# Optimization experiments

Hardware: AMD Instinct MI355X
Metric: run time of the kernel (lower is better)

The kernel has to match this reference:

```python
import jax, jax.numpy as jnp
import numpy as np
import math

B, H, W, CIN = 8, 64, 64, 192
INNER, K, N, P = 384, 2, 32, 64
NHK = INNER // P          # heads per scan direction = 6
NH = K * NHK              # total heads = 12
HID = 4 * CIN

def _silu(v):
    return v * jax.nn.sigmoid(v)

def setup_inputs() -> dict:
    key = jax.random.key(0)
    ks = jax.random.split(key, 12)
    x = jax.random.normal(ks[0], (B, H, W, CIN), jnp.float32)
    W_in = jax.random.normal(ks[1], (2 * INNER, CIN), jnp.float32) * 0.02
    conv_w = jax.random.normal(ks[2], (INNER, 1, 3, 3), jnp.float32) * 0.1
    conv_b = jnp.zeros((INNER,), jnp.float32)
    x_proj_weight = jax.random.normal(ks[3], (K, 2 * N + NHK, INNER), jnp.float32) * 0.02
    A_logs = jnp.log(jax.random.uniform(ks[4], (NH,), jnp.float32, 1.0, 16.0))
    Ds = jnp.ones((NH,), jnp.float32)
    u = jax.random.uniform(ks[5], (NH,), jnp.float32)
    dt = jnp.exp(u * (math.log(0.1) - math.log(0.001)) + math.log(0.001))
    dt = jnp.clip(dt, 1e-4, None)
    dt_bias = dt + jnp.log(-jnp.expm1(-dt))
    init_states = jnp.zeros((NH, P, N), jnp.float32)
    W_out = jax.random.normal(ks[6], (CIN, INNER), jnp.float32) * 0.02
    W1 = jax.random.normal(ks[7], (HID, CIN), jnp.float32) * 0.02
    b1 = jnp.zeros((HID,), jnp.float32)
    W2 = jax.random.normal(ks[8], (CIN, HID), jnp.float32) * 0.02
    b2 = jnp.zeros((CIN,), jnp.float32)
    return dict(x=x, W_in=W_in, conv_w=conv_w, conv_b=conv_b, x_proj_weight=x_proj_weight,
                A_logs=A_logs, Ds=Ds, dt_bias=dt_bias, init_states=init_states,
                W_out=W_out, W1=W1, b1=b1, W2=W2, b2=b2)

def reference(x, W_in, conv_w, conv_b, x_proj_weight, A_logs, Ds, dt_bias,
              init_states, W_out, W1, b1, W2, b2):
    Bb, Hh, Ww, Cin = x.shape
    L = Hh * Ww
    inner = W_in.shape[0] // 2
    shortcut = x
    # norm1 is identity (norm=None). in_proj (no bias), split into x and gate z
    xz = jnp.einsum('bhwc,dc->bhwd', x, W_in)
    xl, z = jnp.split(xz, 2, axis=-1)
    # depthwise conv (NCHW) + SiLU
    xc = jnp.transpose(xl, (0, 3, 1, 2))
    xc = jax.lax.conv_general_dilated(xc, conv_w, (1, 1), 'SAME',
                                      feature_group_count=inner,
                                      dimension_numbers=('NCHW', 'OIHW', 'NCHW'))
    xc = _silu(xc + conv_b[None, :, None, None])
    # cross scan: row-major and transposed (W-major) flattenings
    xs = jnp.stack([xc.reshape(Bb, inner, L),
                    jnp.transpose(xc, (0, 1, 3, 2)).reshape(Bb, inner, L)], axis=1)  # (B,K,inner,L)
    # project to B, C, dt per direction
    BCdt = jnp.einsum('bkdl,kcd->blkc', xs, x_proj_weight)  # (B,L,K,2N+NHK)
    Bs = BCdt[..., :N]                     # (B,L,K,N)
    Cs = BCdt[..., N:2 * N]                # (B,L,K,N)
    dt = BCdt[..., 2 * N:].reshape(Bb, L, NH)
    xh = jnp.transpose(xs, (0, 3, 1, 2)).reshape(Bb, L, NH, P)  # heads: k-major
    # Mamba2 selective scan (dt_softplus with bias)
    dt = jax.nn.softplus(dt + dt_bias)     # (B,L,NH)
    A = -jnp.exp(A_logs)                   # (NH,)
    da = jnp.exp(dt * A)                   # (B,L,NH)
    dtx = dt[..., None] * xh               # (B,L,NH,P)
    Bh = jnp.repeat(Bs, NHK, axis=2)       # (B,L,NH,N) group -> heads
    Ch = jnp.repeat(Cs, NHK, axis=2)
    h0 = jnp.broadcast_to(init_states, (Bb,) + init_states.shape)  # (B,NH,P,N)
    def step(h, inp):
        da_t, dtx_t, B_t, C_t = inp
        h = da_t[..., None, None] * h + dtx_t[..., None] * B_t[:, :, None, :]
        y_t = jnp.einsum('bhpn,bhn->bhp', h, C_t)
        return h, y_t
    _, ys = jax.lax.scan(step, h0, (jnp.moveaxis(da, 1, 0), jnp.moveaxis(dtx, 1, 0),
                                    jnp.moveaxis(Bh, 1, 0), jnp.moveaxis(Ch, 1, 0)))
    y = jnp.moveaxis(ys, 0, 1) + Ds[None, None, :, None] * xh  # (B,L,NH,P)
    out_y = jnp.transpose(y.reshape(Bb, L, K, inner), (0, 2, 3, 1))  # (B,K,inner,L)
    # scan_proj: undo each direction's flattening and sum
    y0 = out_y[:, 0].reshape(Bb, inner, Hh, Ww)
    y1 = jnp.transpose(out_y[:, 1].reshape(Bb, inner, Ww, Hh), (0, 1, 3, 2))
    yr = jnp.transpose((y0 + y1).reshape(Bb, inner, L), (0, 2, 1)).reshape(Bb, Hh, Ww, inner)
    # gate, out_proj, residual, MLP branch (dense is identity since in==out)
    yg = yr * _silu(z)
    out = shortcut + jnp.einsum('bhwd,cd->bhwc', yg, W_out)
    h1 = _silu(jnp.einsum('...c,dc->...d', out, W1) + b1)
    mlp = jnp.einsum('...d,cd->...c', h1, W2) + b2
    return out + mlp
```

## Files before the change

### kernel.cpp

```cpp
#include <hip/hip_runtime.h>
#include <math.h>

#define BB 8
#define HH 64
#define WW 64
#define CIN 192
#define INNER 384
#define LL 4096
#define NSTATE 32
#define PDIM 64
#define NHK 6
#define NHEADS 12
#define HID 768
#define CPROJ 70
#define QC 64
#define NC 64

#define WS_XLZ   0u
#define WS_XC    50331648u
#define WS_Y1    75497472u
#define WS_BCBF  100663296u
#define WS_DTRAW 109051904u
#define WS_DTV   119013376u
#define WS_CUMS  120586240u
#define WS_SHB   122159104u
#define WS_Y0    147324928u
#define WS_XBF   172490752u
#define WS_WINB  185073664u
#define WS_WPADB 185368576u
#define WS_WOUTB 185565184u
#define WS_W1B   185761792u
#define WS_W2B   186056704u
#define WS_REQ   186449920u

typedef __attribute__((ext_vector_type(8))) short short8;
typedef __attribute__((ext_vector_type(4))) float f32x4;

__device__ __forceinline__ float silu_f(float x) { return x / (1.f + __expf(-x)); }

__device__ __forceinline__ unsigned short f2bf(float f) {
    unsigned u = __float_as_uint(f);
    u += 0x7fffu + ((u >> 16) & 1u);
    return (unsigned short)(u >> 16);
}
__device__ __forceinline__ float bf2f(unsigned short u) {
    return __uint_as_float(((unsigned)u) << 16);
}

template<int EPI, int TRANSA>
__global__ __launch_bounds__(256)
void gemm_bf16(const unsigned short* __restrict__ A, const unsigned short* __restrict__ Wt,
               const float* __restrict__ bias, const float* __restrict__ res,
               float* __restrict__ Cf, unsigned short* __restrict__ Cb,
               int Kd, int ldc, int nmax)
{
    __shared__ __align__(16) short Als[128 * 64];
    __shared__ __align__(16) short Bls[128 * 64];
    const int tid = threadIdx.x;
    const int m0 = blockIdx.x * 128;
    const int n0 = blockIdx.y * 128;
    const int lane = tid & 63;
    const int wv = tid >> 6;
    const int wm = (wv >> 1) << 6;
    const int wn = (wv & 1) << 6;

    const unsigned short* gA[4];
    const unsigned short* gB[4];
    int lw[4];
    #pragma unroll
    for (int c = 0; c < 4; ++c) {
        const int idx = c * 256 + tid;
        const int row = idx >> 3;
        const int kb  = idx & 7;
        const int sb  = kb ^ (row & 7);
        lw[c] = row * 64 + sb * 8;
        size_t arow;
        const int mm = m0 + row;
        if (TRANSA) {
            const int bq = mm >> 12, lq = mm & 4095;
            arow = ((size_t)bq << 12) + (size_t)(((lq & 63) << 6) + (lq >> 6));
        } else {
            arow = (size_t)mm;
        }
        gA[c] = A + arow * Kd + kb * 8;
        gB[c] = Wt + (size_t)(n0 + row) * Kd + kb * 8;
    }

    f32x4 acc[4][4];
    #pragma unroll
    for (int i = 0; i < 4; ++i)
        #pragma unroll
        for (int j = 0; j < 4; ++j) acc[i][j] = (f32x4){0.f, 0.f, 0.f, 0.f};

    const int NT = Kd >> 6;
    short8 pA[4], pB[4];
    #pragma unroll
    for (int c = 0; c < 4; ++c) {
        pA[c] = *(const short8*)(gA[c]);
        pB[c] = *(const short8*)(gB[c]);
    }
    for (int kt = 0; kt < NT; ++kt) {
        __syncthreads();
        #pragma unroll
        for (int c = 0; c < 4; ++c) {
            *(short8*)&Als[lw[c]] = pA[c];
            *(short8*)&Bls[lw[c]] = pB[c];
        }
        __syncthreads();
        if (kt + 1 < NT) {
            #pragma unroll
            for (int c = 0; c < 4; ++c) {
                pA[c] = *(const short8*)(gA[c] + (kt + 1) * 64);
                pB[c] = *(const short8*)(gB[c] + (kt + 1) * 64);
            }
        }
        #pragma unroll
        for (int ks = 0; ks < 2; ++ks) {
            short8 af[4], bfr[4];
            #pragma unroll
            for (int r = 0; r < 4; ++r) {
                const int rowa = wm + r * 16 + (lane & 15);
                const int rowb = wn + r * 16 + (lane & 15);
                const int kb = ks * 4 + (lane >> 4);
                af[r]  = *(const short8*)&Als[rowa * 64 + ((kb ^ (rowa & 7)) << 3)];
                bfr[r] = *(const short8*)&Bls[rowb * 64 + ((kb ^ (rowb & 7)) << 3)];
            }
            #pragma unroll
            for (int mr = 0; mr < 4; ++mr)
                #pragma unroll
                for (int nr = 0; nr < 4; ++nr)
                    acc[mr][nr] = __builtin_amdgcn_mfma_f32_16x16x32_bf16(af[mr], bfr[nr], acc[mr][nr], 0, 0, 0);
        }
    }
    #pragma unroll
    for (int mr = 0; mr < 4; ++mr) {
        #pragma unroll
        for (int nr = 0; nr < 4; ++nr) {
            const int n = n0 + wn + nr * 16 + (lane & 15);
            if (n >= nmax) continue;
            const int mb = m0 + wm + mr * 16 + ((lane >> 4) << 2);
            #pragma unroll
            for (int q = 0; q < 4; ++q) {
                const size_t off = (size_t)(mb + q) * ldc + n;
                float v = acc[mr][nr][q];
                if (EPI == 0) { Cf[off] = v; }
                else if (EPI == 1) { v = silu_f(v + bias[n]); Cb[off] = f2bf(v); }
                else if (EPI == 2) { v += bias[n] + res[off]; Cf[off] = v; }
                else if (EPI == 3) { v += res[off]; Cf[off] = v; Cb[off] = f2bf(v); }
                else if (EPI == 4) { Cb[off] = f2bf(v); }
                else if (EPI == 5) {
                    if (n < 64) Cb[(size_t)(mb + q) * 128 + n] = f2bf(v);
                    else        Cf[(size_t)(mb + q) * 12 + (n - 64)] = v;
                }
            }
        }
    }
}

__global__ __launch_bounds__(256)
void cvt_kernel(const float* __restrict__ src, unsigned short* __restrict__ dst, int n)
{
    const int i = blockIdx.x * 256 + threadIdx.x;
    if (i < n) dst[i] = f2bf(src[i]);
}

__global__ __launch_bounds__(256)
void cvt_weights_kernel(const float* __restrict__ W_in, const float* __restrict__ W1,
                        const float* __restrict__ xpw, const float* __restrict__ W_out,
                        const float* __restrict__ W2,
                        unsigned short* __restrict__ Winb, unsigned short* __restrict__ W1b,
                        unsigned short* __restrict__ wpadb, unsigned short* __restrict__ Woutb,
                        unsigned short* __restrict__ W2b)
{
    int i = blockIdx.x * 256 + threadIdx.x;
    if (i < 147456) { Winb[i] = f2bf(W_in[i]); return; }
    i -= 147456;
    if (i < 147456) { W1b[i] = f2bf(W1[i]); return; }
    i -= 147456;
    if (i < 98304) {
        const int d = i % 384;
        const int rr = (i / 384) & 127;
        const int k = i / 49152;
        wpadb[i] = (rr < CPROJ) ? f2bf(xpw[((size_t)k * CPROJ + rr) * 384 + d]) : (unsigned short)0;
        return;
    }
    i -= 98304;
    if (i < 98304) {
        const int rr = i / 384;
        Woutb[i] = (rr < CIN) ? f2bf(W_out[i]) : (unsigned short)0;
        return;
    }
    i -= 98304;
    if (i < 196608) {
        const int rr = i / 768;
        W2b[i] = (rr < CIN) ? f2bf(W2[i]) : (unsigned short)0;
    }
}

__global__ __launch_bounds__(256)
void conv_dw_kernel(const unsigned short* __restrict__ xlz, const float* __restrict__ cw,
                    const float* __restrict__ cb, unsigned short* __restrict__ xcbf)
{
    const int t = blockIdx.x * 256 + threadIdx.x;
    const int dv = t % 48;
    int r = t / 48;
    const int j  = r & 63;  r >>= 6;
    const int ib = r & 7;   r >>= 3;
    const int b  = r;
    const int d0 = dv * 8;
    const int i0 = ib * 8;

    float wreg[72];
    {
        const float4* w4 = (const float4*)(cw + d0 * 9);
        #pragma unroll
        for (int u = 0; u < 18; ++u) {
            const float4 v = w4[u];
            wreg[4*u+0]=v.x; wreg[4*u+1]=v.y; wreg[4*u+2]=v.z; wreg[4*u+3]=v.w;
        }
    }
    float bias[8];
    {
        const float4 b0 = *(const float4*)(cb + d0);
        const float4 b1 = *(const float4*)(cb + d0 + 4);
        bias[0]=b0.x; bias[1]=b0.y; bias[2]=b0.z; bias[3]=b0.w;
        bias[4]=b1.x; bias[5]=b1.y; bias[6]=b1.z; bias[7]=b1.w;
    }

    const unsigned short* base = xlz + ((size_t)b << 12) * 768 + d0;
    const int jok[3] = { (j - 1 >= 0), 1, (j + 1 < WW) };

    unsigned rm[3][4], r0[3][4], rp[3][4];
    #pragma unroll
    for (int cj = 0; cj < 3; ++cj) {
        uint4 vm = make_uint4(0,0,0,0), v0 = make_uint4(0,0,0,0);
        if (jok[cj]) {
            if (i0 - 1 >= 0) vm = *(const uint4*)(base + (size_t)((i0-1) * 64 + j - 1 + cj) * 768);
            v0 = *(const uint4*)(base + (size_t)(i0 * 64 + j - 1 + cj) * 768);
        }
        rm[cj][0]=vm.x; rm[cj][1]=vm.y; rm[cj][2]=vm.z; rm[cj][3]=vm.w;
        r0[cj][0]=v0.x; r0[cj][1]=v0.y; r0[cj][2]=v0.z; r0[cj][3]=v0.w;
    }

    #pragma unroll
    for (int ii = 0; ii < 8; ++ii) {
        const int i = i0 + ii;
        #pragma unroll
        for (int cj = 0; cj < 3; ++cj) {
            uint4 vp = make_uint4(0,0,0,0);
            if (jok[cj] && (i + 1 < HH))
                vp = *(const uint4*)(base + (size_t)((i+1) * 64 + j - 1 + cj) * 768);
            rp[cj][0]=vp.x; rp[cj][1]=vp.y; rp[cj][2]=vp.z; rp[cj][3]=vp.w;
        }
        float acc[8];
        #pragma unroll
        for (int ch = 0; ch < 8; ++ch) acc[ch] = bias[ch];
        #pragma unroll
        for (int cj = 0; cj < 3; ++cj) {
            #pragma unroll
            for (int w2 = 0; w2 < 4; ++w2) {
                acc[2*w2+0] = fmaf(__uint_as_float(rm[cj][w2] << 16),        wreg[(2*w2+0)*9 + cj],     acc[2*w2+0]);
                acc[2*w2+1] = fmaf(__uint_as_float(rm[cj][w2] & 0xffff0000u), wreg[(2*w2+1)*9 + cj],     acc[2*w2+1]);
                acc[2*w2+0] = fmaf(__uint_as_float(r0[cj][w2] << 16),        wreg[(2*w2+0)*9 + 3 + cj], acc[2*w2+0]);
                acc[2*w2+1] = fmaf(__uint_as_float(r0[cj][w2] & 0xffff0000u), wreg[(2*w2+1)*9 + 3 + cj], acc[2*w2+1]);
                acc[2*w2+0] = fmaf(__uint_as_float(rp[cj][w2] << 16),        wreg[(2*w2+0)*9 + 6 + cj], acc[2*w2+0]);
                acc[2*w2+1] = fmaf(__uint_as_float(rp[cj][w2] & 0xffff0000u), wreg[(2*w2+1)*9 + 6 + cj], acc[2*w2+1]);
            }
        }
        unsigned o[4];
        #pragma unroll
        for (int w2 = 0; w2 < 4; ++w2) {
            const unsigned lo = f2bf(silu_f(acc[2*w2+0]));
            const unsigned hi = f2bf(silu_f(acc[2*w2+1]));
            o[w2] = lo | (hi << 16);
        }
        *(uint4*)(xcbf + ((size_t)(b << 12) + (size_t)(i * 64 + j)) * INNER + d0) =
            make_uint4(o[0], o[1], o[2], o[3]);
        #pragma unroll
        for (int cj = 0; cj < 3; ++cj)
            #pragma unroll
            for (int w2 = 0; w2 < 4; ++w2) {
                rm[cj][w2] = r0[cj][w2];
                r0[cj][w2] = rp[cj][w2];
            }
    }
}

__global__ __launch_bounds__(256)
void dtcums_kernel(const float* __restrict__ dtraw, const float* __restrict__ dt_bias,
                   const float* __restrict__ A_logs,
                   float* __restrict__ dtv, float* __restrict__ cums)
{
    const int w = blockIdx.x * 4 + (threadIdx.x >> 6);
    const int lane = threadIdx.x & 63;
    const int b = w / (NHEADS * NC);
    const int rem = w - b * (NHEADS * NC);
    const int h = rem / NC;
    const int c = rem - h * NC;
    const int k = h / NHK;
    const int hq = h - k * NHK;
    const int l = c * QC + lane;
    const float dtr = dtraw[(((size_t)b * LL + l) * 2 + k) * 6 + hq];
    const float xx = dtr + dt_bias[h];
    const float sp = (xx > 20.f) ? xx : log1pf(expf(xx));
    float s = -expf(A_logs[h]) * sp;
    #pragma unroll
    for (int d = 1; d < 64; d <<= 1) {
        const float o = __shfl_up(s, d);
        if (lane >= d) s += o;
    }
    dtv[((size_t)b * LL + l) * NHEADS + h] = sp;
    cums[((size_t)b * LL + l) * NHEADS + h] = s;
}

__global__ __launch_bounds__(256)
void chunk_state_kernel(const unsigned short* __restrict__ xcbf, const unsigned short* __restrict__ BCbf,
                        const float* __restrict__ dtv, const float* __restrict__ cums,
                        unsigned short* __restrict__ SHb)
{
    __shared__ __align__(16) unsigned short Xb[PDIM][72];
    __shared__ __align__(16) unsigned short Bsc[NSTATE][72];
    __shared__ float cuS[QC], rs[QC];
    const int c = blockIdx.x, h = blockIdx.y, b = blockIdx.z;
    const int k = h / NHK;
    const int dch0 = (h - k * NHK) * PDIM;
    const int tid = threadIdx.x;
    const int lane = tid & 63;
    const int w = tid >> 6;

    #pragma unroll
    for (int r = 0; r < 16; ++r) {
        const int idx = tid + r * 256;
        const int m = idx >> 6, p = idx & 63;
        const int pos = (k == 0) ? (c * QC + m) : (m * QC + c);
        Xb[p][m] = xcbf[(((size_t)b << 12) + pos) * INNER + dch0 + p];
    }
    if (tid < QC)
        cuS[tid] = cums[((size_t)b * LL + c * QC + tid) * NHEADS + h];
    __syncthreads();
    if (tid < QC)
        rs[tid] = dtv[((size_t)b * LL + c * QC + tid) * NHEADS + h] * __expf(cuS[QC-1] - cuS[tid]);
    __syncthreads();
    #pragma unroll
    for (int r = 0; r < 8; ++r) {
        const int idx = tid + r * 256;
        const int m = idx >> 5, n = idx & 31;
        Bsc[n][m] = f2bf(rs[m] * bf2f(BCbf[(((size_t)b * LL + c * QC + m) * 2 + k) * 64 + n]));
    }
    __syncthreads();

    const int rowf = lane & 15;
    const int ko   = lane >> 4;
    f32x4 acc[2] = {{0.f,0.f,0.f,0.f},{0.f,0.f,0.f,0.f}};
    #pragma unroll
    for (int ks = 0; ks < 2; ++ks) {
        const short8 af = *(const short8*)&Xb[w * 16 + rowf][ks * 32 + ko * 8];
        #pragma unroll
        for (int nt = 0; nt < 2; ++nt) {
            const short8 bfr = *(const short8*)&Bsc[nt * 16 + rowf][ks * 32 + ko * 8];
            acc[nt] = __builtin_amdgcn_mfma_f32_16x16x32_bf16(af, bfr, acc[nt], 0, 0, 0);
        }
    }
    unsigned short* base = SHb + ((((size_t)b * NHEADS + h) * NC + c) * PDIM) * NSTATE;
    #pragma unroll
    for (int nt = 0; nt < 2; ++nt) {
        #pragma unroll
        for (int q = 0; q < 4; ++q) {
            const int p = w * 16 + ko * 4 + q;
            base[p * NSTATE + nt * 16 + rowf] = f2bf(acc[nt][q]);
        }
    }
}

__global__ __launch_bounds__(64)
void state_scan_kernel(unsigned short* __restrict__ SHb, const float* __restrict__ cums,
                       const float* __restrict__ init_states)
{
    __shared__ float decays[NC];
    const int g = blockIdx.x;
    const int bh = g >> 2;
    const int quarter = g & 3;
    const int b = bh / NHEADS;
    const int h = bh % NHEADS;
    const int tid = threadIdx.x;
    decays[tid] = __expf(cums[((size_t)b * LL + tid * QC + QC - 1) * NHEADS + h]);
    __syncthreads();
    const int p = quarter * 16 + (tid >> 2);
    const int nb = (tid & 3) * 8;
    float hs[8];
    {
        const float* is = init_states + ((size_t)h * PDIM + p) * NSTATE + nb;
        #pragma unroll
        for (int i = 0; i < 8; ++i) hs[i] = is[i];
    }
    unsigned short* base = SHb + (((size_t)b * NHEADS + h) * NC) * (PDIM * NSTATE) + p * NSTATE + nb;
    for (int c = 0; c < NC; ++c) {
        unsigned short* slot = base + (size_t)c * (PDIM * NSTATE);
        const uint4 sv = *(const uint4*)slot;
        const unsigned ua[4] = {sv.x, sv.y, sv.z, sv.w};
        unsigned o[4];
        #pragma unroll
        for (int w2 = 0; w2 < 4; ++w2)
            o[w2] = (unsigned)f2bf(hs[2*w2]) | ((unsigned)f2bf(hs[2*w2+1]) << 16);
        *(uint4*)slot = make_uint4(o[0], o[1], o[2], o[3]);
        const float dc = decays[c];
        #pragma unroll
        for (int w2 = 0; w2 < 4; ++w2) {
            hs[2*w2+0] = fmaf(dc, hs[2*w2+0], __uint_as_float(ua[w2] << 16));
            hs[2*w2+1] = fmaf(dc, hs[2*w2+1], __uint_as_float(ua[w2] & 0xffff0000u));
        }
    }
}

__global__ __launch_bounds__(256)
void intra_kernel(const unsigned short* __restrict__ xcbf, const unsigned short* __restrict__ BCbf,
                  const float* __restrict__ dtv, const float* __restrict__ cums,
                  const unsigned short* __restrict__ SHb, const float* __restrict__ Ds,
                  unsigned short* __restrict__ y0, unsigned short* __restrict__ y1)
{
    __shared__ __align__(16) unsigned short Bs[QC][40];
    __shared__ __align__(16) unsigned short Cs[QC][40];
    __shared__ __align__(16) unsigned short Hs[PDIM][40];
    __shared__ __align__(16) unsigned short Xb[PDIM][72];
    __shared__ __align__(16) unsigned short Gb[QC][72];
    __shared__ float cuS[QC], dtS[QC], Ei[QC];
    const int c = blockIdx.x, h = blockIdx.y, b = blockIdx.z;
    const int k = h / NHK;
    const int dch0 = (h - k * NHK) * PDIM;
    const int tid = threadIdx.x;
    const int lane = tid & 63;
    const int w = tid >> 6;

    #pragma unroll
    for (int r = 0; r < 16; ++r) {
        const int idx = tid + r * 256;
        const int m = idx >> 6, p = idx & 63;
        const int pos = (k == 0) ? (c * QC + m) : (m * QC + c);
        Xb[p][m] = xcbf[(((size_t)b << 12) + pos) * INNER + dch0 + p];
    }
    #pragma unroll
    for (int r = 0; r < 2; ++r) {
        const int idx = tid + r * 256;
        const int i = idx >> 3, ch = idx & 7;
        const uint4 v = *(const uint4*)(BCbf + (((size_t)b * LL + c * QC + i) * 2 + k) * 64 + ch * 8);
        if (ch < 4) *(uint4*)&Bs[i][ch * 8] = v;
        else        *(uint4*)&Cs[i][(ch - 4) * 8] = v;
    }
    {
        const int p = tid >> 2, ch = tid & 3;
        *(uint4*)&Hs[p][ch * 8] =
            *(const uint4*)(SHb + ((((size_t)b * NHEADS + h) * NC + c) * PDIM + p) * NSTATE + ch * 8);
    }
    if (tid < QC) {
        const size_t o = ((size_t)b * LL + c * QC + tid) * NHEADS + h;
        const float cu = cums[o];
        cuS[tid] = cu;
        dtS[tid] = dtv[o];
        Ei[tid]  = __expf(cu);
    }
    __syncthreads();

    const int rowf = lane & 15;
    const int ko   = lane >> 4;
    const short8 cfrag = *(const short8*)&Cs[w * 16 + rowf][ko * 8];

    f32x4 graw[4];
    #pragma unroll
    for (int mt = 0; mt < 4; ++mt) {
        const short8 bfrag = *(const short8*)&Bs[mt * 16 + rowf][ko * 8];
        graw[mt] = __builtin_amdgcn_mfma_f32_16x16x32_bf16(cfrag, bfrag, (f32x4){0.f,0.f,0.f,0.f}, 0, 0, 0);
    }
    #pragma unroll
    for (int mt = 0; mt < 4; ++mt) {
        const int m = mt * 16 + rowf;
        const float cum = cuS[m];
        const float dtm = dtS[m];
        #pragma unroll
        for (int q = 0; q < 4; ++q) {
            const int i = w * 16 + ko * 4 + q;
            float g = 0.f;
            if (m <= i) g = __expf(fminf(cuS[i] - cum, 0.f)) * dtm * graw[mt][q];
            Gb[i][m] = f2bf(g);
        }
    }
    f32x4 acc[4];
    #pragma unroll
    for (int pt = 0; pt < 4; ++pt) {
        const short8 hfrag = *(const short8*)&Hs[pt * 16 + rowf][ko * 8];
        acc[pt] = __builtin_amdgcn_mfma_f32_16x16x32_bf16(cfrag, hfrag, (f32x4){0.f,0.f,0.f,0.f}, 0, 0, 0);
    }
    const float Dh = Ds[h];
    #pragma unroll
    for (int pt = 0; pt < 4; ++pt) {
        const int p = pt * 16 + rowf;
        #pragma unroll
        for (int q = 0; q < 4; ++q) {
            const int i = w * 16 + ko * 4 + q;
            acc[pt][q] = acc[pt][q] * Ei[i] + Dh * bf2f(Xb[p][i]);
        }
    }
    #pragma unroll
    for (int ks = 0; ks < 2; ++ks) {
        const short8 gfrag = *(const short8*)&Gb[w * 16 + rowf][ks * 32 + ko * 8];
        #pragma unroll
        for (int pt = 0; pt < 4; ++pt) {
            const short8 xfrag = *(const short8*)&Xb[pt * 16 + rowf][ks * 32 + ko * 8];
            acc[pt] = __builtin_amdgcn_mfma_f32_16x16x32_bf16(gfrag, xfrag, acc[pt], 0, 0, 0);
        }
    }
    unsigned short* yk = (k == 0) ? y0 : y1;
    #pragma unroll
    for (int pt = 0; pt < 4; ++pt) {
        const int p = pt * 16 + rowf;
        #pragma unroll
        for (int q = 0; q < 4; ++q) {
            const int i = w * 16 + ko * 4 + q;
            const int pos = (k == 0) ? (c * QC + i) : (i * QC + c);
            yk[(((size_t)b << 12) + pos) * INNER + dch0 + p] = f2bf(acc[pt][q]);
        }
    }
}

__global__ __launch_bounds__(256)
void gate_kernel(const unsigned short* __restrict__ y0, const unsigned short* __restrict__ y1,
                 const unsigned short* __restrict__ xlz, unsigned short* __restrict__ ygbf)
{
    const int t = blockIdx.x * 256 + threadIdx.x;
    const int dv = t % (INNER / 8);
    const int m  = t / (INNER / 8);
    const int d0 = dv * 8;
    const uint4 a = *(const uint4*)(y0 + (size_t)m * INNER + d0);
    const uint4 bv = *(const uint4*)(y1 + (size_t)m * INNER + d0);
    const uint4 zv = *(const uint4*)(xlz + (size_t)m * 768 + INNER + d0);
    const unsigned ua[4] = {a.x, a.y, a.z, a.w};
    const unsigned ub[4] = {bv.x, bv.y, bv.z, bv.w};
    const unsigned uz[4] = {zv.x, zv.y, zv.z, zv.w};
    unsigned o[4];
    #pragma unroll
    for (int w2 = 0; w2 < 4; ++w2) {
        const float ylo = __uint_as_float(ua[w2] << 16) + __uint_as_float(ub[w2] << 16);
        const float yhi = __uint_as_float(ua[w2] & 0xffff0000u) + __uint_as_float(ub[w2] & 0xffff0000u);
        const float zlo = __uint_as_float(uz[w2] << 16);
        const float zhi = __uint_as_float(uz[w2] & 0xffff0000u);
        o[w2] = (unsigned)f2bf(ylo * silu_f(zlo)) | ((unsigned)f2bf(yhi * silu_f(zhi)) << 16);
    }
    *(uint4*)(ygbf + (size_t)m * INNER + d0) = make_uint4(o[0], o[1], o[2], o[3]);
}

__global__ __launch_bounds__(256)
void report_ws_kernel(float* __restrict__ out, int n, float val)
{
    const int e = blockIdx.x * 256 + threadIdx.x;
    if (e < n) out[e] = val;
}

extern "C" void kernel_launch(void* const* d_in, const int* in_sizes, int n_in,
                              void* d_out, int out_size, void* d_ws, size_t ws_size,
                              hipStream_t stream)
{
    const float* x          = (const float*)d_in[0];
    const float* W_in       = (const float*)d_in[1];
    const float* conv_w     = (const float*)d_in[2];
    const float* conv_b     = (const float*)d_in[3];
    const float* xpw        = (const float*)d_in[4];
    const float* A_logs     = (const float*)d_in[5];
    const float* Ds         = (const float*)d_in[6];
    const float* dt_bias    = (const float*)d_in[7];
    const float* init_states= (const float*)d_in[8];
    const float* W_out      = (const float*)d_in[9];
    const float* W1         = (const float*)d_in[10];
    const float* b1         = (const float*)d_in[11];
    const float* W2         = (const float*)d_in[12];
    const float* b2         = (const float*)d_in[13];
    float* out = (float*)d_out;

    if (ws_size < (size_t)WS_REQ) {
        const float mib = (float)((double)ws_size / 1048576.0);
        report_ws_kernel<<<(out_size + 255) / 256, 256, 0, stream>>>(out, out_size, mib);
        return;
    }

    char* ws = (char*)d_ws;
    unsigned short* xlz   = (unsigned short*)(ws + WS_XLZ);
    unsigned short* xc_bf = (unsigned short*)(ws + WS_XC);
    unsigned short* y1    = (unsigned short*)(ws + WS_Y1);
    unsigned short* BCbf  = (unsigned short*)(ws + WS_BCBF);
    float* dtraw = (float*)(ws + WS_DTRAW);
    float* dtv   = (float*)(ws + WS_DTV);
    float* cums  = (float*)(ws + WS_CUMS);
    unsigned short* SHb   = (unsigned short*)(ws + WS_SHB);
    unsigned short* y0    = (unsigned short*)(ws + WS_Y0);
    unsigned short* x_bf  = (unsigned short*)(ws + WS_XBF);
    unsigned short* Winb  = (unsigned short*)(ws + WS_WINB);
    unsigned short* wpadb = (unsigned short*)(ws + WS_WPADB);
    unsigned short* Woutb = (unsigned short*)(ws + WS_WOUTB);
    unsigned short* W1b   = (unsigned short*)(ws + WS_W1B);
    unsigned short* W2b   = (unsigned short*)(ws + WS_W2B);
    unsigned short* yg_bf  = (unsigned short*)(ws + WS_XC);
    unsigned short* out_bf = (unsigned short*)(ws + WS_BCBF);
    unsigned short* h1_bf  = (unsigned short*)(ws + WS_XLZ);

    const int M = BB * LL;

    cvt_kernel<<<(M * CIN + 255) / 256, 256, 0, stream>>>(x, x_bf, M * CIN);
    cvt_weights_kernel<<<(688128 + 255) / 256, 256, 0, stream>>>(W_in, W1, xpw, W_out, W2,
                                                                 Winb, W1b, wpadb, Woutb, W2b);

    gemm_bf16<4,0><<<dim3(M/128, HID/128), 256, 0, stream>>>(x_bf, Winb, nullptr, nullptr, nullptr, xlz, CIN, HID, HID);

    conv_dw_kernel<<<196608 / 256, 256, 0, stream>>>(xlz, conv_w, conv_b, xc_bf);

    gemm_bf16<5,0><<<dim3(M/128, 1), 256, 0, stream>>>(xc_bf, wpadb, nullptr, nullptr, dtraw, BCbf, INNER, 0, CPROJ);
    gemm_bf16<5,1><<<dim3(M/128, 1), 256, 0, stream>>>(xc_bf, wpadb + 128 * INNER, nullptr, nullptr, dtraw + 6, BCbf + 64, INNER, 0, CPROJ);

    dtcums_kernel<<<(BB * NHEADS * NC) / 4, 256, 0, stream>>>(dtraw, dt_bias, A_logs, dtv, cums);

    chunk_state_kernel<<<dim3(NC, NHEADS, BB), 256, 0, stream>>>(xc_bf, BCbf, dtv, cums, SHb);
    state_scan_kernel<<<BB * NHEADS * 4, 64, 0, stream>>>(SHb, cums, init_states);
    intra_kernel<<<dim3(NC, NHEADS, BB), 256, 0, stream>>>(xc_bf, BCbf, dtv, cums, SHb, Ds, y0, y1);

    gate_kernel<<<(M * INNER / 8) / 256, 256, 0, stream>>>(y0, y1, xlz, yg_bf);

    gemm_bf16<3,0><<<dim3(M/128, 2), 256, 0, stream>>>(yg_bf, Woutb, nullptr, x, out, out_bf, INNER, CIN, CIN);

    gemm_bf16<1,0><<<dim3(M/128, HID/128), 256, 0, stream>>>(out_bf, W1b, b1, nullptr, nullptr, h1_bf, CIN, HID, HID);
    gemm_bf16<2,0><<<dim3(M/128, 2), 256, 0, stream>>>(h1_bf, W2b, b2, out, out, nullptr, HID, CIN, CIN);
}
```

Baseline: 241.7 us.

## Fuse input conversion and gating into GEMM A-loads; vectorize chunk X loads

Removes the standalone fp32-to-bf16 conversion of x by converting inside the in_proj GEMM's A-tile load. It also removes the gate kernel: the out_proj GEMM now reads y0, y1 and z directly, summing and SiLU-gating them on load. This saves two full-tensor round trips through memory. Separately, the chunk_state and intra kernels now load X with 16-byte vector reads instead of scalar bf16 reads. The trade-off is that the GEMMs redo the conversion and gating for every N-tile block, and the in_proj GEMM reads twice as many bytes per A element.

```diff
diff --git a/kernel.cpp b/kernel.cpp
--- a/kernel.cpp
+++ b/kernel.cpp
@@ -25,7 +25,6 @@
 #define WS_CUMS  120586240u
 #define WS_SHB   122159104u
 #define WS_Y0    147324928u
-#define WS_XBF   172490752u
 #define WS_WINB  185073664u
 #define WS_WPADB 185368576u
 #define WS_WOUTB 185565184u
@@ -47,11 +46,48 @@
     return __uint_as_float(((unsigned)u) << 16);
 }
 
-template<int EPI, int TRANSA>
+template<int AMODE>
+__device__ __forceinline__ short8 load_a(const void* A, const unsigned short* Ay0,
+                                         const unsigned short* Ay1, const unsigned short* Az,
+                                         int row, int col, int Kd)
+{
+    if constexpr (AMODE == 0) {
+        return *(const short8*)((const unsigned short*)A + (size_t)row * Kd + col);
+    } else if constexpr (AMODE == 1) {
+        const float* Af = (const float*)A + (size_t)row * Kd + col;
+        const float4 v0 = *(const float4*)(Af);
+        const float4 v1 = *(const float4*)(Af + 4);
+        short8 r;
+        r[0]=(short)f2bf(v0.x); r[1]=(short)f2bf(v0.y); r[2]=(short)f2bf(v0.z); r[3]=(short)f2bf(v0.w);
+        r[4]=(short)f2bf(v1.x); r[5]=(short)f2bf(v1.y); r[6]=(short)f2bf(v1.z); r[7]=(short)f2bf(v1.w);
+        return r;
+    } else {
+        const size_t yo = (size_t)row * INNER + col;
+        const uint4 a  = *(const uint4*)(Ay0 + yo);
+        const uint4 bv = *(const uint4*)(Ay1 + yo);
+        const uint4 zv = *(const uint4*)(Az + (size_t)row * 768 + INNER + col);
+        const unsigned ua[4]={a.x,a.y,a.z,a.w}, ub[4]={bv.x,bv.y,bv.z,bv.w}, uz[4]={zv.x,zv.y,zv.z,zv.w};
+        short8 r;
+        #pragma unroll
+        for (int w2 = 0; w2 < 4; ++w2) {
+            const float ylo = __uint_as_float(ua[w2] << 16) + __uint_as_float(ub[w2] << 16);
+            const float yhi = __uint_as_float(ua[w2] & 0xffff0000u) + __uint_as_float(ub[w2] & 0xffff0000u);
+            const float zlo = __uint_as_float(uz[w2] << 16);
+            const float zhi = __uint_as_float(uz[w2] & 0xffff0000u);
+            r[2*w2+0] = (short)f2bf(ylo * silu_f(zlo));
+            r[2*w2+1] = (short)f2bf(yhi * silu_f(zhi));
+        }
+        return r;
+    }
+}
+
+template<int EPI, int TRANSA, int AMODE>
 __global__ __launch_bounds__(256)
-void gemm_bf16(const unsigned short* __restrict__ A, const unsigned short* __restrict__ Wt,
+void gemm_bf16(const void* __restrict__ A, const unsigned short* __restrict__ Wt,
                const float* __restrict__ bias, const float* __restrict__ res,
                float* __restrict__ Cf, unsigned short* __restrict__ Cb,
+               const unsigned short* __restrict__ Ay0, const unsigned short* __restrict__ Ay1,
+               const unsigned short* __restrict__ Az,
                int Kd, int ldc, int nmax)
 {
     __shared__ __align__(16) short Als[128 * 64];
@@ -64,7 +100,7 @@
     const int wm = (wv >> 1) << 6;
     const int wn = (wv & 1) << 6;
 
-    const unsigned short* gA[4];
+    int am[4], ac[4];
     const unsigned short* gB[4];
     int lw[4];
     #pragma unroll
@@ -74,15 +110,16 @@
         const int kb  = idx & 7;
         const int sb  = kb ^ (row & 7);
         lw[c] = row * 64 + sb * 8;
-        size_t arow;
+        int arow;
         const int mm = m0 + row;
         if (TRANSA) {
             const int bq = mm >> 12, lq = mm & 4095;
-            arow = ((size_t)bq << 12) + (size_t)(((lq & 63) << 6) + (lq >> 6));
+            arow = (bq << 12) + (((lq & 63) << 6) + (lq >> 6));
         } else {
-            arow = (size_t)mm;
-        }
-        gA[c] = A + arow * Kd + kb * 8;
+            arow = mm;
+        }
+        am[c] = arow;
+        ac[c] = kb * 8;
         gB[c] = Wt + (size_t)(n0 + row) * Kd + kb * 8;
     }
 
@@ -96,7 +133,7 @@
     short8 pA[4], pB[4];
     #pragma unroll
     for (int c = 0; c < 4; ++c) {
-        pA[c] = *(const short8*)(gA[c]);
+        pA[c] = load_a<AMODE>(A, Ay0, Ay1, Az, am[c], ac[c], Kd);
         pB[c] = *(const short8*)(gB[c]);
     }
     for (int kt = 0; kt < NT; ++kt) {
@@ -110,7 +147,7 @@
         if (kt + 1 < NT) {
             #pragma unroll
             for (int c = 0; c < 4; ++c) {
-                pA[c] = *(const short8*)(gA[c] + (kt + 1) * 64);
+                pA[c] = load_a<AMODE>(A, Ay0, Ay1, Az, am[c], ac[c] + (kt + 1) * 64, Kd);
                 pB[c] = *(const short8*)(gB[c] + (kt + 1) * 64);
             }
         }
@@ -158,13 +195,6 @@
 }
 
 __global__ __launch_bounds__(256)
-void cvt_kernel(const float* __restrict__ src, unsigned short* __restrict__ dst, int n)
-{
-    const int i = blockIdx.x * 256 + threadIdx.x;
-    if (i < n) dst[i] = f2bf(src[i]);
-}
-
-__global__ __launch_bounds__(256)
 void cvt_weights_kernel(const float* __restrict__ W_in, const float* __restrict__ W1,
                         const float* __restrict__ xpw, const float* __restrict__ W_out,
                         const float* __restrict__ W2,
@@ -329,11 +359,17 @@
     const int w = tid >> 6;
 
     #pragma unroll
-    for (int r = 0; r < 16; ++r) {
-        const int idx = tid + r * 256;
-        const int m = idx >> 6, p = idx & 63;
+    for (int r2 = 0; r2 < 2; ++r2) {
+        const int idx = tid + r2 * 256;
+        const int m = idx >> 3, pg = idx & 7;
         const int pos = (k == 0) ? (c * QC + m) : (m * QC + c);
-        Xb[p][m] = xcbf[(((size_t)b << 12) + pos) * INNER + dch0 + p];
+        const uint4 v = *(const uint4*)(xcbf + (((size_t)b << 12) + pos) * INNER + dch0 + pg * 8);
+        const unsigned ua[4] = {v.x, v.y, v.z, v.w};
+        #pragma unroll
+        for (int e2 = 0; e2 < 4; ++e2) {
+            Xb[pg * 8 + 2*e2 + 0][m] = (unsigned short)(ua[e2] & 0xffffu);
+            Xb[pg * 8 + 2*e2 + 1][m] = (unsigned short)(ua[e2] >> 16);
+        }
     }
     if (tid < QC)
         cuS[tid] = cums[((size_t)b * LL + c * QC + tid) * NHEADS + h];
@@ -432,11 +468,17 @@
     const int w = tid >> 6;
 
     #pragma unroll
-    for (int r = 0; r < 16; ++r) {
-        const int idx = tid + r * 256;
-        const int m = idx >> 6, p = idx & 63;
+    for (int r2 = 0; r2 < 2; ++r2) {
+        const int idx = tid + r2 * 256;
+        const int m = idx >> 3, pg = idx & 7;
         const int pos = (k == 0) ? (c * QC + m) : (m * QC + c);
-        Xb[p][m] = xcbf[(((size_t)b << 12) + pos) * INNER + dch0 + p];
+        const uint4 v = *(const uint4*)(xcbf + (((size_t)b << 12) + pos) * INNER + dch0 + pg * 8);
+        const unsigned ua[4] = {v.x, v.y, v.z, v.w};
+        #pragma unroll
+        for (int e2 = 0; e2 < 4; ++e2) {
+            Xb[pg * 8 + 2*e2 + 0][m] = (unsigned short)(ua[e2] & 0xffffu);
+            Xb[pg * 8 + 2*e2 + 1][m] = (unsigned short)(ua[e2] >> 16);
+        }
     }
     #pragma unroll
     for (int r = 0; r < 2; ++r) {
@@ -519,32 +561,6 @@
             yk[(((size_t)b << 12) + pos) * INNER + dch0 + p] = f2bf(acc[pt][q]);
         }
     }
-}
-
-__global__ __launch_bounds__(256)
-void gate_kernel(const unsigned short* __restrict__ y0, const unsigned short* __restrict__ y1,
-                 const unsigned short* __restrict__ xlz, unsigned short* __restrict__ ygbf)
-{
-    const int t = blockIdx.x * 256 + threadIdx.x;
-    const int dv = t % (INNER / 8);
-    const int m  = t / (INNER / 8);
-    const int d0 = dv * 8;
-    const uint4 a = *(const uint4*)(y0 + (size_t)m * INNER + d0);
-    const uint4 bv = *(const uint4*)(y1 + (size_t)m * INNER + d0);
-    const uint4 zv = *(const uint4*)(xlz + (size_t)m * 768 + INNER + d0);
-    const unsigned ua[4] = {a.x, a.y, a.z, a.w};
-    const unsigned ub[4] = {bv.x, bv.y, bv.z, bv.w};
-    const unsigned uz[4] = {zv.x, zv.y, zv.z, zv.w};
-    unsigned o[4];
-    #pragma unroll
-    for (int w2 = 0; w2 < 4; ++w2) {
-        const float ylo = __uint_as_float(ua[w2] << 16) + __uint_as_float(ub[w2] << 16);
-        const float yhi = __uint_as_float(ua[w2] & 0xffff0000u) + __uint_as_float(ub[w2] & 0xffff0000u);
-        const float zlo = __uint_as_float(uz[w2] << 16);
-        const float zhi = __uint_as_float(uz[w2] & 0xffff0000u);
-        o[w2] = (unsigned)f2bf(ylo * silu_f(zlo)) | ((unsigned)f2bf(yhi * silu_f(zhi)) << 16);
-    }
-    *(uint4*)(ygbf + (size_t)m * INNER + d0) = make_uint4(o[0], o[1], o[2], o[3]);
 }
 
 __global__ __launch_bounds__(256)
@@ -590,28 +606,28 @@
     float* cums  = (float*)(ws + WS_CUMS);
     unsigned short* SHb   = (unsigned short*)(ws + WS_SHB);
     unsigned short* y0    = (unsigned short*)(ws + WS_Y0);
-    unsigned short* x_bf  = (unsigned short*)(ws + WS_XBF);
     unsigned short* Winb  = (unsigned short*)(ws + WS_WINB);
     unsigned short* wpadb = (unsigned short*)(ws + WS_WPADB);
     unsigned short* Woutb = (unsigned short*)(ws + WS_WOUTB);
     unsigned short* W1b   = (unsigned short*)(ws + WS_W1B);
     unsigned short* W2b   = (unsigned short*)(ws + WS_W2B);
-    unsigned short* yg_bf  = (unsigned short*)(ws + WS_XC);
     unsigned short* out_bf = (unsigned short*)(ws + WS_BCBF);
     unsigned short* h1_bf  = (unsigned short*)(ws + WS_XLZ);
 
     const int M = BB * LL;
 
-    cvt_kernel<<<(M * CIN + 255) / 256, 256, 0, stream>>>(x, x_bf, M * CIN);
     cvt_weights_kernel<<<(688128 + 255) / 256, 256, 0, stream>>>(W_in, W1, xpw, W_out, W2,
                                                                  Winb, W1b, wpadb, Woutb, W2b);
 
-    gemm_bf16<4,0><<<dim3(M/128, HID/128), 256, 0, stream>>>(x_bf, Winb, nullptr, nullptr, nullptr, xlz, CIN, HID, HID);
+    gemm_bf16<4,0,1><<<dim3(M/128, HID/128), 256, 0, stream>>>(x, Winb, nullptr, nullptr, nullptr, xlz,
+                                                               nullptr, nullptr, nullptr, CIN, HID, HID);
 
     conv_dw_kernel<<<196608 / 256, 256, 0, stream>>>(xlz, conv_w, conv_b, xc_bf);
 
-    gemm_bf16<5,0><<<dim3(M/128, 1), 256, 0, stream>>>(xc_bf, wpadb, nullptr, nullptr, dtraw, BCbf, INNER, 0, CPROJ);
-    gemm_bf16<5,1><<<dim3(M/128, 1), 256, 0, stream>>>(xc_bf, wpadb + 128 * INNER, nullptr, nullptr, dtraw + 6, BCbf + 64, INNER, 0, CPROJ);
+    gemm_bf16<5,0,0><<<dim3(M/128, 1), 256, 0, stream>>>(xc_bf, wpadb, nullptr, nullptr, dtraw, BCbf,
+                                                         nullptr, nullptr, nullptr, INNER, 0, CPROJ);
+    gemm_bf16<5,1,0><<<dim3(M/128, 1), 256, 0, stream>>>(xc_bf, wpadb + 128 * INNER, nullptr, nullptr, dtraw + 6, BCbf + 64,
+                                                         nullptr, nullptr, nullptr, INNER, 0, CPROJ);
 
     dtcums_kernel<<<(BB * NHEADS * NC) / 4, 256, 0, stream>>>(dtraw, dt_bias, A_logs, dtv, cums);
 
@@ -619,10 +635,11 @@
     state_scan_kernel<<<BB * NHEADS * 4, 64, 0, stream>>>(SHb, cums, init_states);
     intra_kernel<<<dim3(NC, NHEADS, BB), 256, 0, stream>>>(xc_bf, BCbf, dtv, cums, SHb, Ds, y0, y1);
 
-    gate_kernel<<<(M * INNER / 8) / 256, 256, 0, stream>>>(y0, y1, xlz, yg_bf);
-
-    gemm_bf16<3,0><<<dim3(M/128, 2), 256, 0, stream>>>(yg_bf, Woutb, nullptr, x, out, out_bf, INNER, CIN, CIN);
-
-    gemm_bf16<1,0><<<dim3(M/128, HID/128), 256, 0, stream>>>(out_bf, W1b, b1, nullptr, nullptr, h1_bf, CIN, HID, HID);
-    gemm_bf16<2,0><<<dim3(M/128, 2), 256, 0, stream>>>(h1_bf, W2b, b2, out, out, nullptr, HID, CIN, CIN);
-}
+    gemm_bf16<3,0,2><<<dim3(M/128, 2), 256, 0, stream>>>(nullptr, Woutb, nullptr, x, out, out_bf,
+                                                         y0, y1, xlz, INNER, CIN, CIN);
+
+    gemm_bf16<1,0,0><<<dim3(M/128, HID/128), 256, 0, stream>>>(out_bf, W1b, b1, nullptr, nullptr, h1_bf,
+                                                               nullptr, nullptr, nullptr, CIN, HID, HID);
+    gemm_bf16<2,0,0><<<dim3(M/128, 2), 256, 0, stream>>>(h1_bf, W2b, b2, out, out, nullptr,
+                                                         nullptr, nullptr, nullptr, HID, CIN, CIN);
+}
```

Result: no change. 244.5 us (+1.2%).
